# Kernel tuning notes

Hardware: AMD Instinct MI355X
Metric: run time of the kernel (lower is better)

The kernel has to match this reference:

```python
import jax, jax.numpy as jnp
import numpy as np
import math

N = 4_194_304
EPS = 1e-07
CENTER_WEIGHT = 2.0
SIZE_WEIGHT = 1.0


def _make_boxes(kxy, kwh):
    # valid xyxy boxes: top-left in [0,600), width/height in [1,41)
    xy = jax.random.uniform(kxy, (N, 2), dtype=jnp.float32) * 600.0
    wh = jax.random.uniform(kwh, (N, 2), dtype=jnp.float32) * 40.0 + 1.0
    return jnp.concatenate([xy, xy + wh], axis=1)


def setup_inputs() -> dict:
    key = jax.random.key(0)
    k1, k2, k3, k4 = jax.random.split(key, 4)
    return {
        "pred_boxes": _make_boxes(k1, k2),
        "target_boxes": _make_boxes(k3, k4),
    }


def reference(pred_boxes, target_boxes):
    # Only the diagonal of the NxN pairwise CIoU tensors is used by the
    # original module, so compute the matched-pair terms directly (same math).
    px1, py1, px2, py2 = (pred_boxes[:, i] for i in range(4))
    tx1, ty1, tx2, ty2 = (target_boxes[:, i] for i in range(4))

    inter_w = jnp.clip(jnp.minimum(px2, tx2) - jnp.maximum(px1, tx1), 0.0)
    inter_h = jnp.clip(jnp.minimum(py2, ty2) - jnp.maximum(py1, ty1), 0.0)
    inter = inter_w * inter_h
    p_area = (px2 - px1) * (py2 - py1)
    t_area = (tx2 - tx1) * (ty2 - ty1)
    iou = inter / (p_area + t_area - inter + EPS)

    pcx, pcy = (px1 + px2) * 0.5, (py1 + py2) * 0.5
    tcx, tcy = (tx1 + tx2) * 0.5, (ty1 + ty2) * 0.5
    center_dist_sq = (pcx - tcx) ** 2 + (pcy - tcy) ** 2

    c_w = jnp.maximum(px2, tx2) - jnp.minimum(px1, tx1)
    c_h = jnp.maximum(py2, ty2) - jnp.minimum(py1, ty1)
    c_diag_sq = c_w ** 2 + c_h ** 2 + EPS  # bbox_iou adds eps here

    iou_term = 1.0 - iou
    # forward() adds eps again on top of c_diag_sq's eps (faithful to source)
    center_term = center_dist_sq / (c_diag_sq + EPS)

    pw, ph = px2 - px1, py2 - py1
    tw, th = tx2 - tx1, ty2 - ty1
    size_term = ((pw - tw) / (tw + EPS)) ** 2 + ((ph - th) / (th + EPS)) ** 2

    loss = iou_term + CENTER_WEIGHT * center_term + SIZE_WEIGHT * size_term
    return jnp.mean(loss)
```

## Files before the change

### kernel.cpp

```cpp
#include <hip/hip_runtime.h>


#define EPSF 1e-7f
#define UNROLL 4
#define BLOCK 256

__device__ __forceinline__ float fast_rcp(float x) {
    return __builtin_amdgcn_rcpf(x);
}

__device__ __forceinline__ float wave_block_reduce(float acc, float* lds_ws) {
    #pragma unroll
    for (int off = 32; off > 0; off >>= 1)
        acc += __shfl_down(acc, off, 64);
    const int lane = threadIdx.x & 63;
    const int wave = threadIdx.x >> 6;
    if (lane == 0) lds_ws[wave] = acc;
    __syncthreads();
    float s = 0.f;
    if (threadIdx.x == 0) {
        const int nwaves = blockDim.x >> 6;
        for (int w = 0; w < nwaves; ++w) s += lds_ws[w];
    }
    return s;
}

__device__ __forceinline__ float ciou_elem(float4 p, float4 t) {
    const float px1 = p.x, py1 = p.y, px2 = p.z, py2 = p.w;
    const float tx1 = t.x, ty1 = t.y, tx2 = t.z, ty2 = t.w;

    float iw = fminf(px2, tx2) - fmaxf(px1, tx1);
    float ih = fminf(py2, ty2) - fmaxf(py1, ty1);
    iw = fmaxf(iw, 0.f);
    ih = fmaxf(ih, 0.f);
    const float inter  = iw * ih;
    const float pw = px2 - px1, ph = py2 - py1;
    const float tw = tx2 - tx1, th = ty2 - ty1;
    const float p_area = pw * ph;
    const float t_area = tw * th;
    const float iou = inter * fast_rcp(p_area + t_area - inter + EPSF);

    const float dcx = 0.5f * ((px1 + px2) - (tx1 + tx2));
    const float dcy = 0.5f * ((py1 + py2) - (ty1 + ty2));
    const float center_dist_sq = dcx * dcx + dcy * dcy;
    const float cw = fmaxf(px2, tx2) - fminf(px1, tx1);
    const float ch = fmaxf(py2, ty2) - fminf(py1, ty1);
    const float c_diag_sq = cw * cw + ch * ch + EPSF;
    const float center_term = center_dist_sq * fast_rcp(c_diag_sq + EPSF);

    const float sw = (pw - tw) * fast_rcp(tw + EPSF);
    const float sh = (ph - th) * fast_rcp(th + EPSF);
    const float size_term = sw * sw + sh * sh;

    return (1.f - iou) + 2.f * center_term + size_term;
}

__global__ __launch_bounds__(BLOCK) void ciou_partial_kernel(
        const float4* __restrict__ pred,
        const float4* __restrict__ targ,
        float* __restrict__ partial, int n) {
    const int base = blockIdx.x * (BLOCK * UNROLL) + threadIdx.x;

    float4 p[UNROLL], t[UNROLL];
    bool valid[UNROLL];
    #pragma unroll
    for (int u = 0; u < UNROLL; ++u) {
        const int idx = base + u * BLOCK;
        valid[u] = idx < n;
        const int safe = valid[u] ? idx : 0;
        p[u] = pred[safe];
        t[u] = targ[safe];
    }

    float acc0 = 0.f, acc1 = 0.f;
    #pragma unroll
    for (int u = 0; u < UNROLL; u += 2) {
        if (valid[u])     acc0 += ciou_elem(p[u],     t[u]);
        if (valid[u + 1]) acc1 += ciou_elem(p[u + 1], t[u + 1]);
    }
    float acc = acc0 + acc1;

    __shared__ float lds_ws[BLOCK / 64];
    const float blk = wave_block_reduce(acc, lds_ws);
    if (threadIdx.x == 0) partial[blockIdx.x] = blk;
}

__global__ __launch_bounds__(BLOCK) void ciou_final_kernel(
        const float* __restrict__ partial, int nparts,
        float* __restrict__ out, float inv_n) {
    float acc = 0.f;
    for (int i = threadIdx.x; i < nparts; i += blockDim.x)
        acc += partial[i];
    __shared__ float lds_ws[BLOCK / 64];
    const float s = wave_block_reduce(acc, lds_ws);
    if (threadIdx.x == 0) out[0] = s * inv_n;
}

extern "C" void kernel_launch(void* const* d_in, const int* in_sizes, int n_in,
                              void* d_out, int out_size, void* d_ws, size_t ws_size,
                              hipStream_t stream) {
    const float4* pred = (const float4*)d_in[0];
    const float4* targ = (const float4*)d_in[1];
    float* out = (float*)d_out;
    float* partial = (float*)d_ws;

    const int n = in_sizes[0] / 4;
    const int per_block = BLOCK * UNROLL;
    const int grid = (n + per_block - 1) / per_block;

    ciou_partial_kernel<<<grid, BLOCK, 0, stream>>>(pred, targ, partial, n);
    ciou_final_kernel<<<1, BLOCK, 0, stream>>>(partial, grid, out, 1.0f / (float)n);
}
```

Measured before the change: 31.43 us.

## Fuse final reduction into main kernel via atomics and last-block completion

```diff
diff --git a/kernel.cpp b/kernel.cpp
--- a/kernel.cpp
+++ b/kernel.cpp
@@ -2,27 +2,11 @@
 
 
 #define EPSF 1e-7f
-#define UNROLL 4
+#define UNROLL 8
 #define BLOCK 256
 
 __device__ __forceinline__ float fast_rcp(float x) {
     return __builtin_amdgcn_rcpf(x);
-}
-
-__device__ __forceinline__ float wave_block_reduce(float acc, float* lds_ws) {
-    #pragma unroll
-    for (int off = 32; off > 0; off >>= 1)
-        acc += __shfl_down(acc, off, 64);
-    const int lane = threadIdx.x & 63;
-    const int wave = threadIdx.x >> 6;
-    if (lane == 0) lds_ws[wave] = acc;
-    __syncthreads();
-    float s = 0.f;
-    if (threadIdx.x == 0) {
-        const int nwaves = blockDim.x >> 6;
-        for (int w = 0; w < nwaves; ++w) s += lds_ws[w];
-    }
-    return s;
 }
 
 __device__ __forceinline__ float ciou_elem(float4 p, float4 t) {
@@ -55,19 +39,19 @@
     return (1.f - iou) + 2.f * center_term + size_term;
 }
 
-__global__ __launch_bounds__(BLOCK) void ciou_partial_kernel(
+__global__ __launch_bounds__(BLOCK) void ciou_fused_kernel(
         const float4* __restrict__ pred,
         const float4* __restrict__ targ,
-        float* __restrict__ partial, int n) {
+        float* __restrict__ ws,
+        float* __restrict__ out,
+        int n, float inv_n) {
     const int base = blockIdx.x * (BLOCK * UNROLL) + threadIdx.x;
 
     float4 p[UNROLL], t[UNROLL];
-    bool valid[UNROLL];
     #pragma unroll
     for (int u = 0; u < UNROLL; ++u) {
         const int idx = base + u * BLOCK;
-        valid[u] = idx < n;
-        const int safe = valid[u] ? idx : 0;
+        const int safe = idx < n ? idx : 0;
         p[u] = pred[safe];
         t[u] = targ[safe];
     }
@@ -75,25 +59,37 @@
     float acc0 = 0.f, acc1 = 0.f;
     #pragma unroll
     for (int u = 0; u < UNROLL; u += 2) {
-        if (valid[u])     acc0 += ciou_elem(p[u],     t[u]);
-        if (valid[u + 1]) acc1 += ciou_elem(p[u + 1], t[u + 1]);
+        const int i0 = base + u * BLOCK;
+        const int i1 = i0 + BLOCK;
+        if (i0 < n) acc0 += ciou_elem(p[u],     t[u]);
+        if (i1 < n) acc1 += ciou_elem(p[u + 1], t[u + 1]);
     }
     float acc = acc0 + acc1;
 
+    #pragma unroll
+    for (int off = 32; off > 0; off >>= 1)
+        acc += __shfl_down(acc, off, 64);
+
     __shared__ float lds_ws[BLOCK / 64];
-    const float blk = wave_block_reduce(acc, lds_ws);
-    if (threadIdx.x == 0) partial[blockIdx.x] = blk;
-}
+    const int lane = threadIdx.x & 63;
+    const int wave = threadIdx.x >> 6;
+    if (lane == 0) lds_ws[wave] = acc;
+    __syncthreads();
 
-__global__ __launch_bounds__(BLOCK) void ciou_final_kernel(
-        const float* __restrict__ partial, int nparts,
-        float* __restrict__ out, float inv_n) {
-    float acc = 0.f;
-    for (int i = threadIdx.x; i < nparts; i += blockDim.x)
-        acc += partial[i];
-    __shared__ float lds_ws[BLOCK / 64];
-    const float s = wave_block_reduce(acc, lds_ws);
-    if (threadIdx.x == 0) out[0] = s * inv_n;
+    if (threadIdx.x == 0) {
+        float blk = 0.f;
+        #pragma unroll
+        for (int w = 0; w < BLOCK / 64; ++w) blk += lds_ws[w];
+
+        atomicAdd(&ws[0], blk);
+        __threadfence();
+        unsigned* cnt = (unsigned*)(ws + 1);
+        const unsigned old = atomicAdd(cnt, 1u);
+        if (old == gridDim.x - 1) {
+            const float total = atomicAdd(&ws[0], 0.0f);
+            out[0] = total * inv_n;
+        }
+    }
 }
 
 extern "C" void kernel_launch(void* const* d_in, const int* in_sizes, int n_in,
@@ -102,12 +98,13 @@
     const float4* pred = (const float4*)d_in[0];
     const float4* targ = (const float4*)d_in[1];
     float* out = (float*)d_out;
-    float* partial = (float*)d_ws;
+    float* ws = (float*)d_ws;
 
     const int n = in_sizes[0] / 4;
     const int per_block = BLOCK * UNROLL;
     const int grid = (n + per_block - 1) / per_block;
 
-    ciou_partial_kernel<<<grid, BLOCK, 0, stream>>>(pred, targ, partial, n);
-    ciou_final_kernel<<<1, BLOCK, 0, stream>>>(partial, grid, out, 1.0f / (float)n);
+    hipMemsetAsync(d_ws, 0, 2 * sizeof(float), stream);
+    ciou_fused_kernel<<<grid, BLOCK, 0, stream>>>(pred, targ, ws, out, n,
+                                                  1.0f / (float)n);
 }
```

New measurement: 93.16 us. 196% more time.
